# Optimization experiments

Measured on AMD Instinct MI355X. Metric: run time of the kernel, lower is better.

## Reference

```python
import jax, jax.numpy as jnp
import numpy as np

VOCAB = 32000
EMB = 256
DEC = 1024
ENC = 1024  # 2 * encoder hidden (bi-directional)
B = 128
S = 512


def setup_inputs() -> dict:
    key = jax.random.key(0)
    ks = jax.random.split(key, 16)
    s = 0.02
    return {
        "inputs": jax.random.randint(ks[0], (B, 1), 0, VOCAB),
        "decoder_hidden": jax.random.normal(ks[1], (B, DEC), jnp.float32),
        "encoder_output": jax.random.normal(ks[2], (B, S, ENC), jnp.float32),
        "emb": jax.random.normal(ks[3], (VOCAB, EMB), jnp.float32) * s,
        "W1": jax.random.normal(ks[4], (ENC, DEC), jnp.float32) * s,
        "b1": jnp.zeros((DEC,), jnp.float32),
        "W2": jax.random.normal(ks[5], (DEC, DEC), jnp.float32) * s,
        "b2": jnp.zeros((DEC,), jnp.float32),
        "Wv": jax.random.normal(ks[6], (DEC, 1), jnp.float32) * s,
        "bv": jnp.zeros((1,), jnp.float32),
        "lstm_k": jax.random.normal(ks[7], (ENC + EMB, 4 * DEC), jnp.float32) * s,
        "lstm_rk": jax.random.normal(ks[8], (DEC, 4 * DEC), jnp.float32) * s,
        "lstm_b": jnp.zeros((4 * DEC,), jnp.float32),
        "fc_W": jax.random.normal(ks[9], (DEC, VOCAB), jnp.float32) * s,
        "fc_b": jnp.zeros((VOCAB,), jnp.float32),
    }


def reference(inputs, decoder_hidden, encoder_output, emb, W1, b1, W2, b2,
              Wv, bv, lstm_k, lstm_rk, lstm_b, fc_W, fc_b):
    # Bahdanau additive attention
    # score: (B, S, 1)
    hidden_proj = decoder_hidden @ W2 + b2                      # (B, DEC)
    score = jnp.tanh(encoder_output @ W1 + b1 + hidden_proj[:, None, :]) @ Wv + bv
    attention_weights = jax.nn.softmax(score, axis=1)           # (B, S, 1)
    context = jnp.sum(attention_weights * encoder_output, axis=1)  # (B, ENC)

    # embedding lookup of the single input token, concat [context, embed]
    x = jnp.concatenate([context, emb[inputs[:, 0]]], axis=-1)  # (B, ENC+EMB)

    # single-step LSTM. Original calls rnn(inputs) with NO initial_state,
    # so h0 = c0 = 0 and the recurrent kernel contributes nothing this step.
    z = x @ lstm_k + lstm_b + jnp.zeros((B, DEC), x.dtype) @ lstm_rk  # (B, 4*DEC)
    i, f, g, o = jnp.split(z, 4, axis=-1)  # keras gate order i,f,c,o
    c = jax.nn.sigmoid(f) * 0.0 + jax.nn.sigmoid(i) * jnp.tanh(g)
    h = jax.nn.sigmoid(o) * jnp.tanh(c)

    logits = h @ fc_W + fc_b                                    # (B, VOCAB)
    return logits, (h, c), attention_weights
```

## Files before the change

kernel.cpp:

```cpp
#include <hip/hip_runtime.h>
#include <hip/hip_bf16.h>

#define VOCAB 32000
#define EMB   256
#define DEC   1024
#define ENC   1024
#define BB    128
#define SS    512
#define MTOT  (BB * SS)
#define XCOLS (ENC + EMB)
#define NG    (4 * DEC)

typedef _Float16 half8  __attribute__((ext_vector_type(8)));
typedef _Float16 half4  __attribute__((ext_vector_type(4)));
typedef float    floatx4 __attribute__((ext_vector_type(4)));

__device__ __forceinline__ float fast_tanh(float x) {
    float e = __builtin_amdgcn_exp2f(x * 2.885390082f);
    return 1.0f - 2.0f * __builtin_amdgcn_rcpf(e + 1.0f);
}
__device__ __forceinline__ float fast_sigmoid(float x) {
    float e = __builtin_amdgcn_exp2f(-x * 1.442695041f);
    return __builtin_amdgcn_rcpf(1.0f + e);
}

__global__ void k_transpose_w1(const float* __restrict__ W1, _Float16* __restrict__ w1t) {
    __shared__ float tile[32][33];
    const int k0 = blockIdx.y * 32, n0 = blockIdx.x * 32;
    const int tx = threadIdx.x, ty = threadIdx.y;
    #pragma unroll
    for (int j = 0; j < 4; ++j)
        tile[ty + j * 8][tx] = W1[(size_t)(k0 + ty + j * 8) * DEC + n0 + tx];
    __syncthreads();
    #pragma unroll
    for (int j = 0; j < 4; ++j)
        w1t[(size_t)(n0 + ty + j * 8) * ENC + k0 + tx] = (_Float16)tile[tx][ty + j * 8];
}

__global__ void k_hidden_proj(const float* __restrict__ dh, const float* __restrict__ W2,
                              const float* __restrict__ b1, const float* __restrict__ b2,
                              float* __restrict__ hp) {
    __shared__ float xs[8 * 1024];
    const int t = threadIdx.x;
    const int n = blockIdx.x * 128 + t;
    const int b0 = blockIdx.y * 8;
    for (int i = t; i < 2048; i += 128)
        ((floatx4*)xs)[i] = ((const floatx4*)(dh + (size_t)b0 * 1024))[i];
    __syncthreads();
    float acc[8] = {0, 0, 0, 0, 0, 0, 0, 0};
    for (int k = 0; k < 1024; ++k) {
        float wval = W2[(size_t)k * 1024 + n];
        #pragma unroll
        for (int j = 0; j < 8; ++j) acc[j] += xs[j * 1024 + k] * wval;
    }
    const float bias = b1[n] + b2[n];
    #pragma unroll
    for (int j = 0; j < 8; ++j) hp[(size_t)(b0 + j) * 1024 + n] = acc[j] + bias;
}

__global__ __launch_bounds__(256) void k_score(
    const float* __restrict__ enc, const _Float16* __restrict__ w1t,
    const float* __restrict__ hp, const float* __restrict__ wv,
    float* __restrict__ scores)
{
    __shared__ _Float16 As[128 * 40];
    __shared__ _Float16 Bs[128 * 40];
    const int n0 = blockIdx.x * 128;
    const int m0 = blockIdx.y * 128;
    const int b  = m0 >> 9;
    const int t = threadIdx.x;
    const int lane = t & 63, w = t >> 6;
    const int wm = (w >> 1) * 64, wn = (w & 1) * 64;
    const int col = lane & 15, q = lane >> 4;

    floatx4 acc[4][4];
    #pragma unroll
    for (int i = 0; i < 4; ++i)
        #pragma unroll
        for (int j = 0; j < 4; ++j) acc[i][j] = (floatx4){0.f, 0.f, 0.f, 0.f};

    const int sr = t >> 1;
    const int sc = (t & 1) * 16;
    const float*    ag = enc + (size_t)(m0 + sr) * ENC + sc;
    const _Float16* bg = w1t + (size_t)(n0 + sr) * ENC + sc;
    _Float16* asw = &As[sr * 40 + sc];
    _Float16* bsw = &Bs[sr * 40 + sc];

    for (int k0 = 0; k0 < ENC; k0 += 32) {
        __syncthreads();
        floatx4 a0 = *(const floatx4*)(ag + k0);
        floatx4 a1 = *(const floatx4*)(ag + k0 + 4);
        floatx4 a2 = *(const floatx4*)(ag + k0 + 8);
        floatx4 a3 = *(const floatx4*)(ag + k0 + 12);
        half8 bv0 = *(const half8*)(bg + k0);
        half8 bv1 = *(const half8*)(bg + k0 + 8);
        half8 ha, hb;
        #pragma unroll
        for (int e = 0; e < 4; ++e) { ha[e] = (_Float16)a0[e]; ha[e + 4] = (_Float16)a1[e]; }
        #pragma unroll
        for (int e = 0; e < 4; ++e) { hb[e] = (_Float16)a2[e]; hb[e + 4] = (_Float16)a3[e]; }
        *(half8*)(asw)     = ha;
        *(half8*)(asw + 8) = hb;
        *(half8*)(bsw)     = bv0;
        *(half8*)(bsw + 8) = bv1;
        __syncthreads();
        half8 af[4], bf[4];
        #pragma unroll
        for (int i = 0; i < 4; ++i)
            af[i] = *(const half8*)(&As[(wm + i * 16 + col) * 40 + q * 8]);
        #pragma unroll
        for (int j = 0; j < 4; ++j)
            bf[j] = *(const half8*)(&Bs[(wn + j * 16 + col) * 40 + q * 8]);
        #pragma unroll
        for (int i = 0; i < 4; ++i)
            #pragma unroll
            for (int j = 0; j < 4; ++j)
                acc[i][j] = __builtin_amdgcn_mfma_f32_16x16x32_f16(af[i], bf[j], acc[i][j], 0, 0, 0);
    }

    float hpv[4], wvv[4];
    #pragma unroll
    for (int j = 0; j < 4; ++j) {
        int n = n0 + wn + j * 16 + col;
        hpv[j] = hp[b * 1024 + n];
        wvv[j] = wv[n];
    }
    #pragma unroll
    for (int i = 0; i < 4; ++i) {
        float rs0 = 0.f, rs1 = 0.f, rs2 = 0.f, rs3 = 0.f;
        #pragma unroll
        for (int j = 0; j < 4; ++j) {
            rs0 += fast_tanh(acc[i][j][0] + hpv[j]) * wvv[j];
            rs1 += fast_tanh(acc[i][j][1] + hpv[j]) * wvv[j];
            rs2 += fast_tanh(acc[i][j][2] + hpv[j]) * wvv[j];
            rs3 += fast_tanh(acc[i][j][3] + hpv[j]) * wvv[j];
        }
        #pragma unroll
        for (int off = 1; off < 16; off <<= 1) {
            rs0 += __shfl_xor(rs0, off);
            rs1 += __shfl_xor(rs1, off);
            rs2 += __shfl_xor(rs2, off);
            rs3 += __shfl_xor(rs3, off);
        }
        if (col == 0) {
            const int mrow = m0 + wm + i * 16 + q * 4;
            atomicAdd(&scores[mrow + 0], rs0);
            atomicAdd(&scores[mrow + 1], rs1);
            atomicAdd(&scores[mrow + 2], rs2);
            atomicAdd(&scores[mrow + 3], rs3);
        }
    }
}

__global__ void k_softmax_emb(const float* __restrict__ scores, const int* __restrict__ tok,
                              const float* __restrict__ emb, float* __restrict__ aw,
                              float* __restrict__ x) {
    const int b = blockIdx.x, t = threadIdx.x;
    float s0 = scores[b * SS + t];
    float s1 = scores[b * SS + 256 + t];
    float mx = fmaxf(s0, s1);
    for (int off = 32; off; off >>= 1) mx = fmaxf(mx, __shfl_xor(mx, off));
    __shared__ float redm[4], reds[4];
    const int w = t >> 6, lane = t & 63;
    if (lane == 0) redm[w] = mx;
    __syncthreads();
    mx = fmaxf(fmaxf(redm[0], redm[1]), fmaxf(redm[2], redm[3]));
    float e0 = exp2f((s0 - mx) * 1.44269504f);
    float e1 = exp2f((s1 - mx) * 1.44269504f);
    float sm = e0 + e1;
    for (int off = 32; off; off >>= 1) sm += __shfl_xor(sm, off);
    if (lane == 0) reds[w] = sm;
    __syncthreads();
    sm = reds[0] + reds[1] + reds[2] + reds[3];
    const float inv = 1.0f / sm;
    aw[b * SS + t]       = e0 * inv;
    aw[b * SS + 256 + t] = e1 * inv;
    x[(size_t)b * XCOLS + ENC + t] = emb[(size_t)tok[b] * EMB + t];
}

__global__ void k_context(const float* __restrict__ enc, const float* __restrict__ aw,
                          float* __restrict__ x) {
    const int b = blockIdx.x >> 2;
    const int e = (blockIdx.x & 3) * 256 + threadIdx.x;
    const float* ep = enc + (size_t)b * SS * ENC + e;
    const float* ap = aw + b * SS;
    float acc = 0.f;
    #pragma unroll 8
    for (int s = 0; s < SS; ++s) acc += ap[s] * ep[(size_t)s * ENC];
    x[(size_t)b * XCOLS + e] = acc;
}

__global__ void k_lstm(const float* __restrict__ x, const float* __restrict__ lk,
                       float* __restrict__ z) {
    __shared__ float xs[8 * XCOLS];
    const int t = threadIdx.x;
    const int n = blockIdx.x * 128 + t;
    const int b0 = blockIdx.y * 8;
    for (int i = t; i < 2560; i += 128)
        ((floatx4*)xs)[i] = ((const floatx4*)(x + (size_t)b0 * XCOLS))[i];
    __syncthreads();
    float acc[8] = {0, 0, 0, 0, 0, 0, 0, 0};
    for (int k = 0; k < XCOLS; ++k) {
        float wval = lk[(size_t)k * NG + n];
        #pragma unroll
        for (int j = 0; j < 8; ++j) acc[j] += xs[j * XCOLS + k] * wval;
    }
    #pragma unroll
    for (int j = 0; j < 8; ++j) z[(size_t)(b0 + j) * NG + n] = acc[j];
}

__global__ void k_gates(const float* __restrict__ z, const float* __restrict__ lb,
                        float* __restrict__ h_out, float* __restrict__ c_out) {
    const int idx = blockIdx.x * 256 + threadIdx.x;
    const int b = idx >> 10, d = idx & 1023;
    const float* zb = z + (size_t)b * NG;
    float iv = zb[d]        + lb[d];
    float gv = zb[d + 2048] + lb[d + 2048];
    float ov = zb[d + 3072] + lb[d + 3072];
    float c = fast_sigmoid(iv) * fast_tanh(gv);
    float h = fast_sigmoid(ov) * fast_tanh(c);
    h_out[idx] = h;
    c_out[idx] = c;
}

__global__ __launch_bounds__(256) void k_fc(
    const float* __restrict__ hsrc, const float* __restrict__ fcW,
    const float* __restrict__ fcb, float* __restrict__ logits)
{
    __shared__ _Float16 As[128 * 40];
    __shared__ _Float16 Bs[128 * 40];
    const int n0 = blockIdx.x * 128;
    const int t = threadIdx.x;
    const int lane = t & 63, w = t >> 6;
    const int wm = (w >> 1) * 64, wn = (w & 1) * 64;
    const int col = lane & 15, q = lane >> 4;

    floatx4 acc[4][4];
    #pragma unroll
    for (int i = 0; i < 4; ++i)
        #pragma unroll
        for (int j = 0; j < 4; ++j) acc[i][j] = (floatx4){0.f, 0.f, 0.f, 0.f};

    const int sr = t >> 1, sc = (t & 1) * 16;
    const float* ag = hsrc + (size_t)sr * 1024 + sc;
    _Float16* asw = &As[sr * 40 + sc];
    const int bn = (t & 31) * 4;
    const int bk = (t >> 5) * 4;

    for (int k0 = 0; k0 < 1024; k0 += 32) {
        __syncthreads();
        floatx4 a0 = *(const floatx4*)(ag + k0);
        floatx4 a1 = *(const floatx4*)(ag + k0 + 4);
        floatx4 a2 = *(const floatx4*)(ag + k0 + 8);
        floatx4 a3 = *(const floatx4*)(ag + k0 + 12);
        half8 ha, hb;
        #pragma unroll
        for (int e = 0; e < 4; ++e) { ha[e] = (_Float16)a0[e]; ha[e + 4] = (_Float16)a1[e]; }
        #pragma unroll
        for (int e = 0; e < 4; ++e) { hb[e] = (_Float16)a2[e]; hb[e + 4] = (_Float16)a3[e]; }
        *(half8*)(asw)     = ha;
        *(half8*)(asw + 8) = hb;
        floatx4 w0 = *(const floatx4*)(fcW + (size_t)(k0 + bk + 0) * VOCAB + n0 + bn);
        floatx4 w1 = *(const floatx4*)(fcW + (size_t)(k0 + bk + 1) * VOCAB + n0 + bn);
        floatx4 w2 = *(const floatx4*)(fcW + (size_t)(k0 + bk + 2) * VOCAB + n0 + bn);
        floatx4 w3 = *(const floatx4*)(fcW + (size_t)(k0 + bk + 3) * VOCAB + n0 + bn);
        #pragma unroll
        for (int c = 0; c < 4; ++c) {
            half4 p = { (_Float16)w0[c], (_Float16)w1[c], (_Float16)w2[c], (_Float16)w3[c] };
            *(half4*)(&Bs[(bn + c) * 40 + bk]) = p;
        }
        __syncthreads();
        half8 af[4], bf[4];
        #pragma unroll
        for (int i = 0; i < 4; ++i)
            af[i] = *(const half8*)(&As[(wm + i * 16 + col) * 40 + q * 8]);
        #pragma unroll
        for (int j = 0; j < 4; ++j)
            bf[j] = *(const half8*)(&Bs[(wn + j * 16 + col) * 40 + q * 8]);
        #pragma unroll
        for (int i = 0; i < 4; ++i)
            #pragma unroll
            for (int j = 0; j < 4; ++j)
                acc[i][j] = __builtin_amdgcn_mfma_f32_16x16x32_f16(af[i], bf[j], acc[i][j], 0, 0, 0);
    }

    float fcbv[4];
    #pragma unroll
    for (int j = 0; j < 4; ++j) fcbv[j] = fcb[n0 + wn + j * 16 + col];
    #pragma unroll
    for (int i = 0; i < 4; ++i)
        #pragma unroll
        for (int j = 0; j < 4; ++j)
            #pragma unroll
            for (int r = 0; r < 4; ++r) {
                const int row = wm + i * 16 + q * 4 + r;
                logits[(size_t)row * VOCAB + n0 + wn + j * 16 + col] = acc[i][j][r] + fcbv[j];
            }
}

extern "C" void kernel_launch(void* const* d_in, const int* in_sizes, int n_in,
                              void* d_out, int out_size, void* d_ws, size_t ws_size,
                              hipStream_t stream) {
    const int*   tok    = (const int*)d_in[0];
    const float* dh     = (const float*)d_in[1];
    const float* enc    = (const float*)d_in[2];
    const float* emb    = (const float*)d_in[3];
    const float* W1     = (const float*)d_in[4];
    const float* b1     = (const float*)d_in[5];
    const float* W2     = (const float*)d_in[6];
    const float* b2     = (const float*)d_in[7];
    const float* Wv     = (const float*)d_in[8];
    const float* lstm_k = (const float*)d_in[10];
    const float* lstm_b = (const float*)d_in[12];
    const float* fc_W   = (const float*)d_in[13];
    const float* fc_b   = (const float*)d_in[14];

    float* out    = (float*)d_out;
    float* logits = out;
    float* h_out  = out + 4096000;
    float* c_out  = out + 4096000 + 131072;
    float* aw     = out + 4096000 + 262144;

    char* ws = (char*)d_ws;
    _Float16* w1t    = (_Float16*)ws;
    float*    hp     = (float*)(ws + 2097152);
    float*    scores = (float*)(ws + 2621440);
    float*    x      = (float*)(ws + 2883584);
    float*    z      = (float*)(ws + 3538944);

    hipMemsetAsync(scores, 0, MTOT * sizeof(float), stream);
    k_transpose_w1<<<dim3(32, 32), dim3(32, 8), 0, stream>>>(W1, w1t);
    k_hidden_proj<<<dim3(8, 16), 128, 0, stream>>>(dh, W2, b1, b2, hp);
    k_score<<<dim3(8, 512), 256, 0, stream>>>(enc, w1t, hp, Wv, scores);
    k_softmax_emb<<<128, 256, 0, stream>>>(scores, tok, emb, aw, x);
    k_context<<<512, 256, 0, stream>>>(enc, aw, x);
    k_lstm<<<dim3(32, 16), 128, 0, stream>>>(x, lstm_k, z);
    k_gates<<<512, 256, 0, stream>>>(z, lstm_b, h_out, c_out);
    k_fc<<<250, 256, 0, stream>>>(h_out, fc_W, fc_b, logits);
}
```

Before: 985.9 us.

## Pre-convert encoder output to fp16 and use direct global-to-LDS loads in score GEMM

Adds a pass that converts the fp32 encoder output to fp16 in workspace, so the score GEMM streams half-precision A tiles and no longer converts in every N-tile block. The new score kernel loads A and B tiles with global_load_lds straight into shared memory and remaps block indices so that blocks sharing an M row-block land on the same XCD for L2 reuse. This costs an extra full read and write of the 256MB encoder tensor, and it only runs when the workspace is large enough.

```diff
diff --git a/kernel.cpp b/kernel.cpp
--- a/kernel.cpp
+++ b/kernel.cpp
@@ -1,5 +1,6 @@
 #include <hip/hip_runtime.h>
 #include <hip/hip_bf16.h>
+#include <stdint.h>
 
 #define VOCAB 32000
 #define EMB   256
@@ -24,6 +25,13 @@
     return __builtin_amdgcn_rcpf(1.0f + e);
 }
 
+__device__ __forceinline__ void gl_lds16(const void* g, void* l) {
+    __builtin_amdgcn_global_load_lds(
+        (const __attribute__((address_space(1))) uint32_t*)g,
+        (__attribute__((address_space(3))) uint32_t*)l,
+        16, 0, 0);
+}
+
 __global__ void k_transpose_w1(const float* __restrict__ W1, _Float16* __restrict__ w1t) {
     __shared__ float tile[32][33];
     const int k0 = blockIdx.y * 32, n0 = blockIdx.x * 32;
@@ -35,6 +43,19 @@
     #pragma unroll
     for (int j = 0; j < 4; ++j)
         w1t[(size_t)(n0 + ty + j * 8) * ENC + k0 + tx] = (_Float16)tile[tx][ty + j * 8];
+}
+
+__global__ void k_convert(const float* __restrict__ src, _Float16* __restrict__ dst) {
+    const int stride = gridDim.x * blockDim.x;
+    const int n8 = (MTOT * ENC) / 8;
+    for (int i = blockIdx.x * blockDim.x + threadIdx.x; i < n8; i += stride) {
+        floatx4 a = ((const floatx4*)src)[2 * i];
+        floatx4 b = ((const floatx4*)src)[2 * i + 1];
+        half8 h;
+        #pragma unroll
+        for (int e = 0; e < 4; ++e) { h[e] = (_Float16)a[e]; h[e + 4] = (_Float16)b[e]; }
+        ((half8*)dst)[i] = h;
+    }
 }
 
 __global__ void k_hidden_proj(const float* __restrict__ dh, const float* __restrict__ W2,
@@ -56,6 +77,91 @@
     const float bias = b1[n] + b2[n];
     #pragma unroll
     for (int j = 0; j < 8; ++j) hp[(size_t)(b0 + j) * 1024 + n] = acc[j] + bias;
+}
+
+__global__ __launch_bounds__(256) void k_score_f16(
+    const _Float16* __restrict__ ench, const _Float16* __restrict__ w1t,
+    const float* __restrict__ hp, const float* __restrict__ wv,
+    float* __restrict__ scores)
+{
+    __shared__ _Float16 As[128 * 32];
+    __shared__ _Float16 Bs[128 * 32];
+    const int g   = blockIdx.x;
+    const int xcd = g & 7;
+    const int n0  = ((g >> 3) & 7) * 128;
+    const int m0  = ((xcd << 6) + (g >> 6)) << 7;
+    const int b   = m0 >> 9;
+    const int t = threadIdx.x;
+    const int lane = t & 63, w = t >> 6;
+    const int wm = (w >> 1) * 64, wn = (w & 1) * 64;
+    const int col = lane & 15, q = lane >> 4;
+
+    floatx4 acc[4][4];
+    #pragma unroll
+    for (int i = 0; i < 4; ++i)
+        #pragma unroll
+        for (int j = 0; j < 4; ++j) acc[i][j] = (floatx4){0.f, 0.f, 0.f, 0.f};
+
+    const int srow = w * 32 + (lane >> 2);
+    const int scol = (lane & 3) * 8;
+    const _Float16* agp = ench + (size_t)(m0 + srow) * ENC + scol;
+    const _Float16* bgp = w1t  + (size_t)(n0 + srow) * ENC + scol;
+    _Float16* alp = &As[(w * 32) * 32];
+    _Float16* blp = &Bs[(w * 32) * 32];
+
+    for (int k0 = 0; k0 < ENC; k0 += 32) {
+        __syncthreads();
+        gl_lds16(agp + k0,                alp);
+        gl_lds16(agp + k0 + (size_t)16 * ENC, alp + 16 * 32);
+        gl_lds16(bgp + k0,                blp);
+        gl_lds16(bgp + k0 + (size_t)16 * ENC, blp + 16 * 32);
+        __syncthreads();
+        half8 af[4], bf[4];
+        #pragma unroll
+        for (int i = 0; i < 4; ++i)
+            af[i] = *(const half8*)(&As[(wm + i * 16 + col) * 32 + q * 8]);
+        #pragma unroll
+        for (int j = 0; j < 4; ++j)
+            bf[j] = *(const half8*)(&Bs[(wn + j * 16 + col) * 32 + q * 8]);
+        #pragma unroll
+        for (int i = 0; i < 4; ++i)
+            #pragma unroll
+            for (int j = 0; j < 4; ++j)
+                acc[i][j] = __builtin_amdgcn_mfma_f32_16x16x32_f16(af[i], bf[j], acc[i][j], 0, 0, 0);
+    }
+
+    float hpv[4], wvv[4];
+    #pragma unroll
+    for (int j = 0; j < 4; ++j) {
+        int n = n0 + wn + j * 16 + col;
+        hpv[j] = hp[b * 1024 + n];
+        wvv[j] = wv[n];
+    }
+    #pragma unroll
+    for (int i = 0; i < 4; ++i) {
+        float rs0 = 0.f, rs1 = 0.f, rs2 = 0.f, rs3 = 0.f;
+        #pragma unroll
+        for (int j = 0; j < 4; ++j) {
+            rs0 += fast_tanh(acc[i][j][0] + hpv[j]) * wvv[j];
+            rs1 += fast_tanh(acc[i][j][1] + hpv[j]) * wvv[j];
+            rs2 += fast_tanh(acc[i][j][2] + hpv[j]) * wvv[j];
+            rs3 += fast_tanh(acc[i][j][3] + hpv[j]) * wvv[j];
+        }
+        #pragma unroll
+        for (int off = 1; off < 16; off <<= 1) {
+            rs0 += __shfl_xor(rs0, off);
+            rs1 += __shfl_xor(rs1, off);
+            rs2 += __shfl_xor(rs2, off);
+            rs3 += __shfl_xor(rs3, off);
+        }
+        if (col == 0) {
+            const int mrow = m0 + wm + i * 16 + q * 4;
+            atomicAdd(&scores[mrow + 0], rs0);
+            atomicAdd(&scores[mrow + 1], rs1);
+            atomicAdd(&scores[mrow + 2], rs2);
+            atomicAdd(&scores[mrow + 3], rs3);
+        }
+    }
 }
 
 __global__ __launch_bounds__(256) void k_score(
@@ -327,11 +433,20 @@
     float*    scores = (float*)(ws + 2621440);
     float*    x      = (float*)(ws + 2883584);
     float*    z      = (float*)(ws + 3538944);
+    _Float16* ench   = (_Float16*)(ws + 6291456);
+
+    const size_t need_fast = 6291456 + (size_t)MTOT * ENC * sizeof(_Float16);
+    const bool fast = ws_size >= need_fast;
 
     hipMemsetAsync(scores, 0, MTOT * sizeof(float), stream);
     k_transpose_w1<<<dim3(32, 32), dim3(32, 8), 0, stream>>>(W1, w1t);
     k_hidden_proj<<<dim3(8, 16), 128, 0, stream>>>(dh, W2, b1, b2, hp);
-    k_score<<<dim3(8, 512), 256, 0, stream>>>(enc, w1t, hp, Wv, scores);
+    if (fast) {
+        k_convert<<<2048, 256, 0, stream>>>(enc, ench);
+        k_score_f16<<<4096, 256, 0, stream>>>(ench, w1t, hp, Wv, scores);
+    } else {
+        k_score<<<dim3(8, 512), 256, 0, stream>>>(enc, w1t, hp, Wv, scores);
+    }
     k_softmax_emb<<<128, 256, 0, stream>>>(scores, tok, emb, aw, x);
     k_context<<<512, 256, 0, stream>>>(enc, aw, x);
     k_lstm<<<dim3(32, 16), 128, 0, stream>>>(x, lstm_k, z);
```

Measured after the change: 975.5 us. About the same (-1.0%).
